# Kernel optimization log

Measured on AMD Instinct MI355X. Metric: run time of the kernel, lower is better.

Reference implementation:

```python
import jax, jax.numpy as jnp
import numpy as np

N, D, E, NCLASS, NLAYERS = 50000, 32, 1600000, 40, 4
DT = 1.0
SCALE = 1.0 / np.sqrt(D)


def _transformer_conv(X, src, dst, Wq, bq, Wk, bk):
    # PyG TransformerConv, heads=1, lin_value=Identity, root_weight=False
    q = X @ Wq + bq                       # [N, D]
    k = X @ Wk + bk                       # [N, D]
    logits = jnp.sum(q[dst] * k[src], axis=-1) * SCALE   # [E]
    # numerically-stable scatter softmax over edges grouped by dst
    m = jax.lax.stop_gradient(jax.ops.segment_max(logits, dst, num_segments=N))
    e = jnp.exp(logits - m[dst])
    s = jax.ops.segment_sum(e, dst, num_segments=N)
    alpha = e / s[dst]                    # [E]
    # weighted scatter-sum aggregation of source features
    return jax.ops.segment_sum(alpha[:, None] * X[src], dst, num_segments=N)


def setup_inputs() -> dict:
    key = jax.random.key(0)
    ks = jax.random.split(key, 8)
    x = jax.random.normal(ks[0], (N, D), dtype=jnp.float32)
    edge_index = jax.random.randint(ks[1], (2, E), 0, N, dtype=jnp.int32)
    g = 1.0 / np.sqrt(D)
    Wq = jax.random.normal(ks[2], (D, D), dtype=jnp.float32) * g
    bq = jnp.zeros((D,), dtype=jnp.float32)
    Wk = jax.random.normal(ks[3], (D, D), dtype=jnp.float32) * g
    bk = jnp.zeros((D,), dtype=jnp.float32)
    Wr = jax.random.normal(ks[4], (D, NCLASS), dtype=jnp.float32) * g
    br = jnp.zeros((NCLASS,), dtype=jnp.float32)
    return {"x": x, "edge_index": edge_index, "Wq": Wq, "bq": bq,
            "Wk": Wk, "bk": bk, "Wr": Wr, "br": br}


def reference(x, edge_index, Wq, bq, Wk, bk, Wr, br):
    src, dst = edge_index[0], edge_index[1]   # PyG: row=source j, col=target i
    X = x                                      # emb is Identity; dropout=0 (eval)
    xs = [X]
    for _ in range(NLAYERS):                   # Euler ODE steps, fixed small count
        X = X + DT * (_transformer_conv(X, src, dst, Wq, bq, Wk, bk) - X)
        xs.append(X)
    out = X @ Wr + br                          # [N, NCLASS]
    X_all = jnp.stack(xs, axis=1)              # [N, NLAYERS+1, D]
    return (out, X_all)
```

## Files before the change

### kernel.cpp

```cpp
#include <hip/hip_runtime.h>
#include <hip/hip_fp16.h>
#include <math.h>

#define NN 50000
#define DD 32
#define EE 1600000
#define NCLS 40
#define NLAY 4
#define SCALE_C 0.17677669529663687f
#define EXP2SC  0.2550348710334252f
#define XSTRIDE (DD * (NLAY + 1))
#define CHUNK 128

#define NPB 128
#define NB  391
#define CAP 4608
#define TILE 8192
#define NBLK_SC 196
#define NBLK_PREP 6250

typedef _Float16 f16x2 __attribute__((ext_vector_type(2)));
typedef unsigned int uint;
typedef unsigned short ushort;


__device__ __forceinline__ float fdot2(uint a, uint b, float c) {
#if __has_builtin(__builtin_amdgcn_fdot2)
    return __builtin_amdgcn_fdot2(__builtin_bit_cast(f16x2, a),
                                  __builtin_bit_cast(f16x2, b), c, false);
#else
    float2 af = __half22float2(__builtin_bit_cast(__half2, a));
    float2 bf = __half22float2(__builtin_bit_cast(__half2, b));
    return c + af.x * bf.x + af.y * bf.y;
#endif
}

__device__ __forceinline__ __half2 h2shfl_xor(__half2 v, int off) {
    return __builtin_bit_cast(__half2, __shfl_xor(__builtin_bit_cast(uint, v), off));
}

__global__ __launch_bounds__(256) void g_build(
    const int* __restrict__ src, const int* __restrict__ dst,
    int* __restrict__ bcur, int* __restrict__ packed,
    const float* __restrict__ x,
    const float* __restrict__ Wq, const float* __restrict__ bq,
    const float* __restrict__ Wk, const float* __restrict__ bk,
    float* __restrict__ xall, __half* __restrict__ q16, __half* __restrict__ kx,
    uint* __restrict__ W16p)
{
    int b = blockIdx.x, t = threadIdx.x;
    if (b < NBLK_SC) {
        __shared__ int lhist[NB], gbase[NB], lcur[NB];
        for (int i = t; i < NB; i += 256) lhist[i] = 0;
        __syncthreads();
        int base = b * TILE;
        int es[32], eb[32];
#pragma unroll
        for (int j = 0; j < 32; ++j) {
            int e = base + j * 256 + t;
            if (e < EE) {
                int sv = src[e], dv = dst[e];
                es[j] = sv | ((dv & (NPB - 1)) << 16);
                eb[j] = dv >> 7;
                atomicAdd(&lhist[eb[j]], 1);
            } else eb[j] = -1;
        }
        __syncthreads();
        for (int i = t; i < NB; i += 256) {
            int c = lhist[i];
            gbase[i] = (c > 0) ? atomicAdd(&bcur[i], c) : 0;
            lcur[i] = 0;
        }
        __syncthreads();
#pragma unroll
        for (int j = 0; j < 32; ++j) {
            if (eb[j] >= 0) {
                int r = atomicAdd(&lcur[eb[j]], 1);
                packed[eb[j] * CAP + gbase[eb[j]] + r] = es[j];
            }
        }
    } else if (b < NBLK_SC + NBLK_PREP) {
        __shared__ float sWq[DD * DD], sWk[DD * DD], sbq[DD], sbk[DD];
        for (int i = t; i < DD * DD; i += 256) { sWq[i] = Wq[i]; sWk[i] = Wk[i]; }
        if (t < DD) { sbq[t] = bq[t]; sbk[t] = bk[t]; }
        __syncthreads();
        int tt = (b - NBLK_SC) * 256 + t;
        int n = tt >> 5, j = tt & 31;
        const float* xr = x + n * DD;
        float aq = sbq[j], ak = sbk[j];
#pragma unroll
        for (int i = 0; i < DD; ++i) {
            float xv = xr[i];
            aq += xv * sWq[i * DD + j];
            ak += xv * sWk[i * DD + j];
        }
        float xv = xr[j];
        xall[n * XSTRIDE + j] = xv;
        q16[tt] = __float2half(aq);
        kx[n * 64 + j]      = __float2half(ak);
        kx[n * 64 + 32 + j] = __float2half(xv);
    } else {
        for (int t2 = t; t2 < 1024; t2 += 256) {
            int side = t2 >> 9, rest = t2 & 511, i = rest >> 5, j = rest & 31;
            const float* W = side ? Wk : Wq;
            __half2 h; h.x = __float2half(W[(2 * i) * DD + j]);
            h.y = __float2half(W[(2 * i + 1) * DD + j]);
            W16p[t2] = __builtin_bit_cast(uint, h);
        }
    }
}

__global__ __launch_bounds__(256) void g_bfinal(
    const int* __restrict__ bcur, const int* __restrict__ packed,
    int* __restrict__ rowstart, int* __restrict__ degg,
    ushort* __restrict__ csr_src)
{
    __shared__ int ldeg[NPB], lpre[NPB], lc[NPB];
    int b = blockIdx.x, t = threadIdx.x;
    int cnt = min(bcur[b], CAP);
    int node0 = b << 7;
    int nn = min(NPB, NN - node0);
    if (t < NPB) ldeg[t] = 0;
    __syncthreads();
    const int* pk = packed + b * CAP;
    for (int i = t; i < cnt; i += 256) atomicAdd(&ldeg[pk[i] >> 16], 1);
    __syncthreads();
    if (t < NPB) lpre[t] = ldeg[t];
    __syncthreads();
    for (int off = 1; off < NPB; off <<= 1) {
        int v = 0;
        if (t < NPB && t >= off) v = lpre[t - off];
        __syncthreads();
        if (t < NPB) lpre[t] += v;
        __syncthreads();
    }
    int csrbase = b * CAP;
    if (t < nn) {
        int ex = lpre[t] - ldeg[t];
        rowstart[node0 + t] = csrbase + ex;
        degg[node0 + t] = ldeg[t];
        lc[t] = csrbase + ex;
    }
    __syncthreads();
    for (int i = t; i < cnt; i += 256) {
        int p = pk[i];
        int pos = atomicAdd(&lc[p >> 16], 1);
        csr_src[pos] = (ushort)(p & 0xFFFF);
    }
}

template<int DO_QK>
__global__ __launch_bounds__(256) void g_node(
    const int* __restrict__ rowstart, const int* __restrict__ degg,
    const ushort* __restrict__ csr_src,
    const __half* __restrict__ q16, const uint* __restrict__ kx,
    float* __restrict__ Xnext,
    __half* __restrict__ q16n, uint* __restrict__ kxn,
    const uint* __restrict__ W16p,
    const float* __restrict__ bq, const float* __restrict__ bk)
{
    __shared__ int  sS[4][2][CHUNK];
    __shared__ uint sX[4][2][16];
    int wv   = threadIdx.x >> 6;
    int lane = threadIdx.x & 63;
    int h  = lane >> 5;
    int l5 = lane & 31;
    int g  = l5 >> 2;
    int j  = lane & 3;
    int n = blockIdx.x * 8 + wv * 2 + h;
    int base = rowstart[n];
    int deg  = degg[n];

    uint4 qq = ((const uint4*)(q16 + n * DD))[j];

    float s_part = 0.0f;
    __half2 zero2 = __float2half2_rn(0.0f);
    __half2 a01 = zero2, a23 = zero2, a45 = zero2, a67 = zero2;

    for (int co = 0; co < deg; co += CHUNK) {
        int cdeg = min(CHUNK, deg - co);
        for (int i = l5; i < cdeg; i += 32) sS[wv][h][i] = csr_src[base + co + i];
#pragma unroll 2
        for (int i0 = 0; i0 < cdeg; i0 += 8) {
            int i = i0 + g;
            bool valid = i < cdeg;
            int sn = sS[wv][h][valid ? i : 0];
            const uint4* row = (const uint4*)(kx + sn * 32);
            uint4 kk = row[j];
            uint4 xx = row[4 + j];
            float dotp = fdot2(kk.w, qq.w, fdot2(kk.z, qq.z,
                         fdot2(kk.y, qq.y, fdot2(kk.x, qq.x, 0.0f))));
            dotp += __shfl_xor(dotp, 1);
            dotp += __shfl_xor(dotp, 2);
            dotp = valid ? dotp : -INFINITY;
            float w = exp2f(dotp * EXP2SC);
            s_part += w;
            __half2 wh2 = __float2half2_rn(w);
            a01 = __hfma2(wh2, __builtin_bit_cast(__half2, xx.x), a01);
            a23 = __hfma2(wh2, __builtin_bit_cast(__half2, xx.y), a23);
            a45 = __hfma2(wh2, __builtin_bit_cast(__half2, xx.z), a45);
            a67 = __hfma2(wh2, __builtin_bit_cast(__half2, xx.w), a67);
        }
    }
#pragma unroll
    for (int off = 4; off <= 16; off <<= 1) {
        s_part += __shfl_xor(s_part, off);
        a01 = __hadd2(a01, h2shfl_xor(a01, off));
        a23 = __hadd2(a23, h2shfl_xor(a23, off));
        a45 = __hadd2(a45, h2shfl_xor(a45, off));
        a67 = __hadd2(a67, h2shfl_xor(a67, off));
    }
    float inv = (deg > 0) ? 1.0f / s_part : 0.0f;
    __half2 inv2 = __float2half2_rn(inv);
    __half2 o01 = __hmul2(a01, inv2), o23 = __hmul2(a23, inv2);
    __half2 o45 = __hmul2(a45, inv2), o67 = __hmul2(a67, inv2);

    if (g == 0) {
        float2 f01 = __half22float2(o01), f23 = __half22float2(o23);
        float2 f45 = __half22float2(o45), f67 = __half22float2(o67);
        float4 lo; lo.x = f01.x; lo.y = f01.y; lo.z = f23.x; lo.w = f23.y;
        float4 hi; hi.x = f45.x; hi.y = f45.y; hi.z = f67.x; hi.w = f67.y;
        float* xo = Xnext + n * XSTRIDE + 8 * j;
        *(float4*)xo = lo;
        *(float4*)(xo + 4) = hi;
        if (DO_QK) {
            uint4 st;
            st.x = __builtin_bit_cast(uint, o01); st.y = __builtin_bit_cast(uint, o23);
            st.z = __builtin_bit_cast(uint, o45); st.w = __builtin_bit_cast(uint, o67);
            ((uint4*)(kxn + n * 32))[4 + j] = st;
            sX[wv][h][4 * j + 0] = st.x; sX[wv][h][4 * j + 1] = st.y;
            sX[wv][h][4 * j + 2] = st.z; sX[wv][h][4 * j + 3] = st.w;
        }
    }
    if (DO_QK) {
        int j2 = lane & 31, side = lane >> 5;
        const uint* Wcol = W16p + side * 512;
        float bb = side ? bk[j2] : bq[j2];
#pragma unroll
        for (int hh = 0; hh < 2; ++hh) {
            int nh = blockIdx.x * 8 + wv * 2 + hh;
            float acc = bb;
#pragma unroll
            for (int i = 0; i < 16; ++i)
                acc = fdot2(Wcol[i * 32 + j2], sX[wv][hh][i], acc);
            __half hv = __float2half(acc);
            if (side == 0) q16n[nh * DD + j2] = hv;
            else ((__half*)kxn)[nh * 64 + j2] = hv;
        }
    }
}

__global__ void g_out(const float* __restrict__ Xfin, const float* __restrict__ Wr,
                      const float* __restrict__ br, float* __restrict__ out) {
    __shared__ float sWr[DD * NCLS], sbr[NCLS];
    for (int i = threadIdx.x; i < DD * NCLS; i += blockDim.x) sWr[i] = Wr[i];
    if (threadIdx.x < NCLS) sbr[threadIdx.x] = br[threadIdx.x];
    __syncthreads();
    int t = blockIdx.x * blockDim.x + threadIdx.x;
    if (t >= NN * NCLS) return;
    int n = t / NCLS, c = t % NCLS;
    const float* xr = Xfin + n * XSTRIDE;
    float a = sbr[c];
#pragma unroll
    for (int i = 0; i < DD; ++i) a += xr[i] * sWr[i * NCLS + c];
    out[t] = a;
}

extern "C" void kernel_launch(void* const* d_in, const int* in_sizes, int n_in,
                              void* d_out, int out_size, void* d_ws, size_t ws_size,
                              hipStream_t stream) {
    const float* x  = (const float*)d_in[0];
    const int*   ei = (const int*)d_in[1];
    const int*   src = ei;
    const int*   dst = ei + EE;
    const float* Wq = (const float*)d_in[2];
    const float* bq = (const float*)d_in[3];
    const float* Wk = (const float*)d_in[4];
    const float* bk = (const float*)d_in[5];
    const float* Wr = (const float*)d_in[6];
    const float* br = (const float*)d_in[7];

    float* out  = (float*)d_out;
    float* xall = out + (size_t)NN * NCLS;

    char* wsp = (char*)d_ws;
    __half* q16A = (__half*)wsp;                       wsp += sizeof(__half) * NN * DD;
    __half* q16B = (__half*)wsp;                       wsp += sizeof(__half) * NN * DD;
    uint*   kxA  = (uint*)wsp;                         wsp += sizeof(uint) * NN * 32;
    uint*   kxB  = (uint*)wsp;                         wsp += sizeof(uint) * NN * 32;
    uint*   W16p = (uint*)wsp;                         wsp += sizeof(uint) * 1024;
    int* bcur     = (int*)wsp;                         wsp += sizeof(int) * NB;
    int* rowstart = (int*)wsp;                         wsp += sizeof(int) * NN;
    int* degg     = (int*)wsp;                         wsp += sizeof(int) * NN;
    int* packed   = (int*)wsp;                         wsp += sizeof(int) * NB * CAP;
    ushort* csr_src = (ushort*)wsp;                    wsp += sizeof(ushort) * NB * CAP;

    const int B = 256;

    hipMemsetAsync(bcur, 0, sizeof(int) * NB, stream);
    g_build<<<NBLK_SC + NBLK_PREP + 1, B, 0, stream>>>(
        src, dst, bcur, packed, x, Wq, bq, Wk, bk, xall, q16A, (__half*)kxA, W16p);
    g_bfinal<<<NB, B, 0, stream>>>(bcur, packed, rowstart, degg, csr_src);

    for (int l = 0; l < NLAY; ++l) {
        float* Xnxt = xall + (l + 1) * DD;
        __half* qc = (l & 1) ? q16B : q16A;
        __half* qn = (l & 1) ? q16A : q16B;
        uint*   kc = (l & 1) ? kxB : kxA;
        uint*   kn = (l & 1) ? kxA : kxB;
        if (l < NLAY - 1)
            g_node<1><<<NN / 8, B, 0, stream>>>(rowstart, degg, csr_src, qc, kc,
                                                Xnxt, qn, kn, W16p, bq, bk);
        else
            g_node<0><<<NN / 8, B, 0, stream>>>(rowstart, degg, csr_src, qc, kc,
                                                Xnxt, qn, kn, W16p, bq, bk);
    }

    g_out<<<(NN * NCLS + B - 1) / B, B, 0, stream>>>(xall + NLAY * DD, Wr, br, out);
}
```

Measured before the change: 171.6 us.

## Fuse output projection into last node layer, drop LDS staging, coarsen prep blocks

Removes the separate g_out kernel by computing the final Wr projection in the last g_node launch from the aggregated fp16 features already held in shared memory. Wr is pre-packed into fp16 pairs alongside Wq/Wk. The neighbour loop now reads csr_src directly instead of staging chunks into LDS. The prep blocks each process 8 tiles, which cuts the block count and the repeated shared weight loads. The output logits now come from fp16 features and fp16 weights, so precision is lower than the fp32 g_out it replaces.

```diff
diff --git a/kernel.cpp b/kernel.cpp
--- a/kernel.cpp
+++ b/kernel.cpp
@@ -10,14 +10,13 @@
 #define SCALE_C 0.17677669529663687f
 #define EXP2SC  0.2550348710334252f
 #define XSTRIDE (DD * (NLAY + 1))
-#define CHUNK 128
 
 #define NPB 128
 #define NB  391
 #define CAP 4608
 #define TILE 8192
 #define NBLK_SC 196
-#define NBLK_PREP 6250
+#define NBLK_PREP 782
 
 typedef _Float16 f16x2 __attribute__((ext_vector_type(2)));
 typedef unsigned int uint;
@@ -45,6 +44,7 @@
     const float* __restrict__ x,
     const float* __restrict__ Wq, const float* __restrict__ bq,
     const float* __restrict__ Wk, const float* __restrict__ bk,
+    const float* __restrict__ Wr,
     float* __restrict__ xall, __half* __restrict__ q16, __half* __restrict__ kx,
     uint* __restrict__ W16p)
 {
@@ -84,27 +84,39 @@
         for (int i = t; i < DD * DD; i += 256) { sWq[i] = Wq[i]; sWk[i] = Wk[i]; }
         if (t < DD) { sbq[t] = bq[t]; sbk[t] = bk[t]; }
         __syncthreads();
-        int tt = (b - NBLK_SC) * 256 + t;
-        int n = tt >> 5, j = tt & 31;
-        const float* xr = x + n * DD;
-        float aq = sbq[j], ak = sbk[j];
-#pragma unroll
-        for (int i = 0; i < DD; ++i) {
-            float xv = xr[i];
-            aq += xv * sWq[i * DD + j];
-            ak += xv * sWk[i * DD + j];
-        }
-        float xv = xr[j];
-        xall[n * XSTRIDE + j] = xv;
-        q16[tt] = __float2half(aq);
-        kx[n * 64 + j]      = __float2half(ak);
-        kx[n * 64 + 32 + j] = __float2half(xv);
+        int b2 = b - NBLK_SC;
+#pragma unroll
+        for (int rep = 0; rep < 8; ++rep) {
+            int tt = (b2 * 8 + rep) * 256 + t;
+            if (tt >= NN * DD) break;
+            int n = tt >> 5, j = tt & 31;
+            const float* xr = x + n * DD;
+            float aq = sbq[j], ak = sbk[j];
+#pragma unroll
+            for (int i = 0; i < DD; ++i) {
+                float xv = xr[i];
+                aq += xv * sWq[i * DD + j];
+                ak += xv * sWk[i * DD + j];
+            }
+            float xv = xr[j];
+            xall[n * XSTRIDE + j] = xv;
+            q16[tt] = __float2half(aq);
+            kx[n * 64 + j]      = __float2half(ak);
+            kx[n * 64 + 32 + j] = __float2half(xv);
+        }
     } else {
-        for (int t2 = t; t2 < 1024; t2 += 256) {
-            int side = t2 >> 9, rest = t2 & 511, i = rest >> 5, j = rest & 31;
-            const float* W = side ? Wk : Wq;
-            __half2 h; h.x = __float2half(W[(2 * i) * DD + j]);
-            h.y = __float2half(W[(2 * i + 1) * DD + j]);
+        for (int t2 = t; t2 < 1664; t2 += 256) {
+            __half2 h;
+            if (t2 < 1024) {
+                int side = t2 >> 9, rest = t2 & 511, i = rest >> 5, j = rest & 31;
+                const float* W = side ? Wk : Wq;
+                h.x = __float2half(W[(2 * i) * DD + j]);
+                h.y = __float2half(W[(2 * i + 1) * DD + j]);
+            } else {
+                int idx = t2 - 1024, i = idx / NCLS, c = idx % NCLS;
+                h.x = __float2half(Wr[(2 * i) * NCLS + c]);
+                h.y = __float2half(Wr[(2 * i + 1) * NCLS + c]);
+            }
             W16p[t2] = __builtin_bit_cast(uint, h);
         }
     }
@@ -149,7 +161,7 @@
     }
 }
 
-template<int DO_QK>
+template<int DO_QK, int DO_OUT>
 __global__ __launch_bounds__(256) void g_node(
     const int* __restrict__ rowstart, const int* __restrict__ degg,
     const ushort* __restrict__ csr_src,
@@ -157,9 +169,9 @@
     float* __restrict__ Xnext,
     __half* __restrict__ q16n, uint* __restrict__ kxn,
     const uint* __restrict__ W16p,
-    const float* __restrict__ bq, const float* __restrict__ bk)
+    const float* __restrict__ bq, const float* __restrict__ bk,
+    const float* __restrict__ br, float* __restrict__ outp)
 {
-    __shared__ int  sS[4][2][CHUNK];
     __shared__ uint sX[4][2][16];
     int wv   = threadIdx.x >> 6;
     int lane = threadIdx.x & 63;
@@ -176,31 +188,28 @@
     float s_part = 0.0f;
     __half2 zero2 = __float2half2_rn(0.0f);
     __half2 a01 = zero2, a23 = zero2, a45 = zero2, a67 = zero2;
-
-    for (int co = 0; co < deg; co += CHUNK) {
-        int cdeg = min(CHUNK, deg - co);
-        for (int i = l5; i < cdeg; i += 32) sS[wv][h][i] = csr_src[base + co + i];
+    int dm1 = deg - 1;
+
 #pragma unroll 2
-        for (int i0 = 0; i0 < cdeg; i0 += 8) {
-            int i = i0 + g;
-            bool valid = i < cdeg;
-            int sn = sS[wv][h][valid ? i : 0];
-            const uint4* row = (const uint4*)(kx + sn * 32);
-            uint4 kk = row[j];
-            uint4 xx = row[4 + j];
-            float dotp = fdot2(kk.w, qq.w, fdot2(kk.z, qq.z,
-                         fdot2(kk.y, qq.y, fdot2(kk.x, qq.x, 0.0f))));
-            dotp += __shfl_xor(dotp, 1);
-            dotp += __shfl_xor(dotp, 2);
-            dotp = valid ? dotp : -INFINITY;
-            float w = exp2f(dotp * EXP2SC);
-            s_part += w;
-            __half2 wh2 = __float2half2_rn(w);
-            a01 = __hfma2(wh2, __builtin_bit_cast(__half2, xx.x), a01);
-            a23 = __hfma2(wh2, __builtin_bit_cast(__half2, xx.y), a23);
-            a45 = __hfma2(wh2, __builtin_bit_cast(__half2, xx.z), a45);
-            a67 = __hfma2(wh2, __builtin_bit_cast(__half2, xx.w), a67);
-        }
+    for (int i0 = 0; i0 < deg; i0 += 8) {
+        int i = i0 + g;
+        bool valid = i < deg;
+        int sn = (int)csr_src[base + min(i, dm1)];
+        const uint4* row = (const uint4*)(kx + sn * 32);
+        uint4 kk = row[j];
+        uint4 xx = row[4 + j];
+        float dotp = fdot2(kk.w, qq.w, fdot2(kk.z, qq.z,
+                     fdot2(kk.y, qq.y, fdot2(kk.x, qq.x, 0.0f))));
+        dotp += __shfl_xor(dotp, 1);
+        dotp += __shfl_xor(dotp, 2);
+        dotp = valid ? dotp : -INFINITY;
+        float w = exp2f(dotp * EXP2SC);
+        s_part += w;
+        __half2 wh2 = __float2half2_rn(w);
+        a01 = __hfma2(wh2, __builtin_bit_cast(__half2, xx.x), a01);
+        a23 = __hfma2(wh2, __builtin_bit_cast(__half2, xx.y), a23);
+        a45 = __hfma2(wh2, __builtin_bit_cast(__half2, xx.z), a45);
+        a67 = __hfma2(wh2, __builtin_bit_cast(__half2, xx.w), a67);
     }
 #pragma unroll
     for (int off = 4; off <= 16; off <<= 1) {
@@ -223,14 +232,12 @@
         float* xo = Xnext + n * XSTRIDE + 8 * j;
         *(float4*)xo = lo;
         *(float4*)(xo + 4) = hi;
-        if (DO_QK) {
-            uint4 st;
-            st.x = __builtin_bit_cast(uint, o01); st.y = __builtin_bit_cast(uint, o23);
-            st.z = __builtin_bit_cast(uint, o45); st.w = __builtin_bit_cast(uint, o67);
-            ((uint4*)(kxn + n * 32))[4 + j] = st;
-            sX[wv][h][4 * j + 0] = st.x; sX[wv][h][4 * j + 1] = st.y;
-            sX[wv][h][4 * j + 2] = st.z; sX[wv][h][4 * j + 3] = st.w;
-        }
+        uint4 st;
+        st.x = __builtin_bit_cast(uint, o01); st.y = __builtin_bit_cast(uint, o23);
+        st.z = __builtin_bit_cast(uint, o45); st.w = __builtin_bit_cast(uint, o67);
+        if (DO_QK) ((uint4*)(kxn + n * 32))[4 + j] = st;
+        sX[wv][h][4 * j + 0] = st.x; sX[wv][h][4 * j + 1] = st.y;
+        sX[wv][h][4 * j + 2] = st.z; sX[wv][h][4 * j + 3] = st.w;
     }
     if (DO_QK) {
         int j2 = lane & 31, side = lane >> 5;
@@ -248,22 +255,21 @@
             else ((__half*)kxn)[nh * 64 + j2] = hv;
         }
     }
-}
-
-__global__ void g_out(const float* __restrict__ Xfin, const float* __restrict__ Wr,
-                      const float* __restrict__ br, float* __restrict__ out) {
-    __shared__ float sWr[DD * NCLS], sbr[NCLS];
-    for (int i = threadIdx.x; i < DD * NCLS; i += blockDim.x) sWr[i] = Wr[i];
-    if (threadIdx.x < NCLS) sbr[threadIdx.x] = br[threadIdx.x];
-    __syncthreads();
-    int t = blockIdx.x * blockDim.x + threadIdx.x;
-    if (t >= NN * NCLS) return;
-    int n = t / NCLS, c = t % NCLS;
-    const float* xr = Xfin + n * XSTRIDE;
-    float a = sbr[c];
-#pragma unroll
-    for (int i = 0; i < DD; ++i) a += xr[i] * sWr[i * NCLS + c];
-    out[t] = a;
+    if (DO_OUT) {
+        const uint* Wr16 = W16p + 1024;
+        int c = lane;
+#pragma unroll
+        for (int hh = 0; hh < 2; ++hh) {
+            int nh = blockIdx.x * 8 + wv * 2 + hh;
+            if (c < NCLS) {
+                float acc = br[c];
+#pragma unroll
+                for (int i = 0; i < 16; ++i)
+                    acc = fdot2(Wr16[i * NCLS + c], sX[wv][hh][i], acc);
+                outp[nh * NCLS + c] = acc;
+            }
+        }
+    }
 }
 
 extern "C" void kernel_launch(void* const* d_in, const int* in_sizes, int n_in,
@@ -288,7 +294,7 @@
     __half* q16B = (__half*)wsp;                       wsp += sizeof(__half) * NN * DD;
     uint*   kxA  = (uint*)wsp;                         wsp += sizeof(uint) * NN * 32;
     uint*   kxB  = (uint*)wsp;                         wsp += sizeof(uint) * NN * 32;
-    uint*   W16p = (uint*)wsp;                         wsp += sizeof(uint) * 1024;
+    uint*   W16p = (uint*)wsp;                         wsp += sizeof(uint) * 2048;
     int* bcur     = (int*)wsp;                         wsp += sizeof(int) * NB;
     int* rowstart = (int*)wsp;                         wsp += sizeof(int) * NN;
     int* degg     = (int*)wsp;                         wsp += sizeof(int) * NN;
@@ -299,7 +305,7 @@
 
     hipMemsetAsync(bcur, 0, sizeof(int) * NB, stream);
     g_build<<<NBLK_SC + NBLK_PREP + 1, B, 0, stream>>>(
-        src, dst, bcur, packed, x, Wq, bq, Wk, bk, xall, q16A, (__half*)kxA, W16p);
+        src, dst, bcur, packed, x, Wq, bq, Wk, bk, Wr, xall, q16A, (__half*)kxA, W16p);
     g_bfinal<<<NB, B, 0, stream>>>(bcur, packed, rowstart, degg, csr_src);
 
     for (int l = 0; l < NLAY; ++l) {
@@ -309,12 +315,10 @@
         uint*   kc = (l & 1) ? kxB : kxA;
         uint*   kn = (l & 1) ? kxA : kxB;
         if (l < NLAY - 1)
-            g_node<1><<<NN / 8, B, 0, stream>>>(rowstart, degg, csr_src, qc, kc,
-                                                Xnxt, qn, kn, W16p, bq, bk);
+            g_node<1, 0><<<NN / 8, B, 0, stream>>>(rowstart, degg, csr_src, qc, kc,
+                                                   Xnxt, qn, kn, W16p, bq, bk, br, out);
         else
-            g_node<0><<<NN / 8, B, 0, stream>>>(rowstart, degg, csr_src, qc, kc,
-                                                Xnxt, qn, kn, W16p, bq, bk);
-    }
-
-    g_out<<<(NN * NCLS + B - 1) / B, B, 0, stream>>>(xall + NLAY * DD, Wr, br, out);
-}
+            g_node<0, 1><<<NN / 8, B, 0, stream>>>(rowstart, degg, csr_src, qc, kc,
+                                                   Xnxt, qn, kn, W16p, bq, bk, br, out);
+    }
+}
```

Measured after the change: 165.0 us. 3.8% less time.
